# Optimization experiments

Measured on AMD Instinct MI355X. Metric: run time of the kernel, lower is better.

## Reference

```python
import jax, jax.numpy as jnp
import numpy as np

N_HEAD = 16


def setup_inputs() -> dict:
    key = jax.random.key(0)
    ks = jax.random.split(key, 5)
    B, L, C = 2, 2048, 1024
    s = 0.02
    return {
        "x": jax.random.normal(ks[0], (B, L, C), dtype=jnp.float32),
        "attn_mask": jnp.ones((B, L), dtype=jnp.int64),
        "Wq": jax.random.normal(ks[1], (C, C), dtype=jnp.float32) * s,
        "Wk": jax.random.normal(ks[2], (C, C), dtype=jnp.float32) * s,
        "Wv": jax.random.normal(ks[3], (C, C), dtype=jnp.float32) * s,
        "Wp": jax.random.normal(ks[4], (C, C), dtype=jnp.float32) * s,
    }


def reference(x, attn_mask, Wq, Wk, Wv, Wp):
    B, L, C = x.shape
    H = N_HEAD
    D = C // H
    # nn.Linear(bias=False): y = x @ W.T with W of shape (out, in)
    q = (x @ Wq.T).reshape(B, L, H, D).transpose(0, 2, 1, 3)  # (B,H,L,D)
    k = (x @ Wk.T).reshape(B, L, H, D).transpose(0, 2, 1, 3)
    v = (x @ Wv.T).reshape(B, L, H, D).transpose(0, 2, 1, 3)
    att = jnp.einsum("bhqd,bhkd->bhqk", q, k) / jnp.sqrt(jnp.asarray(D, x.dtype))
    causal = jnp.tril(jnp.ones((L, L), dtype=bool))  # (L,L)
    tok = (attn_mask != 0)[:, None, None, :]  # (B,1,1,L) key-side padding mask
    mask = causal[None, None, :, :] & tok
    att = jnp.where(mask, att, -jnp.inf)
    att = jax.nn.softmax(att, axis=-1)
    # dropout p=0.0 (eval): identity
    y = jnp.einsum("bhqk,bhkd->bhqd", att, v)
    y = y.transpose(0, 2, 1, 3).reshape(B, L, C)
    return y @ Wp.T
```

## Files before the change

kernel.cpp:

```cpp
#include <hip/hip_runtime.h>
#include <hip/hip_bf16.h>
#include <cstdint>

typedef _Float16 f16;
typedef _Float16 f16x4 __attribute__((ext_vector_type(4)));
typedef _Float16 f16x8 __attribute__((ext_vector_type(8)));
typedef float f32x4 __attribute__((ext_vector_type(4)));

#define LNEG (-1e30f)
#define EXP2(x) __builtin_amdgcn_exp2f(x)

__device__ __forceinline__ f32x4 mfma16(f16x8 a, f16x8 b, f32x4 c){
    return __builtin_amdgcn_mfma_f32_16x16x32_f16(a, b, c, 0, 0, 0);
}

__global__ __launch_bounds__(256) void cvt5(
    const float* __restrict__ x,  const float* __restrict__ wq,
    const float* __restrict__ wk, const float* __restrict__ wv,
    const float* __restrict__ wp, f16* __restrict__ dst, int nx8)
{
    int i = blockIdx.x * blockDim.x + threadIdx.x;
    const float* src; int off;
    if (i < nx8){ src = x; off = i; }
    else {
        int j = i - nx8;
        int s = j >> 17;
        off = j & 131071;
        src = (s == 0) ? wq : (s == 1) ? wk : (s == 2) ? wv : wp;
    }
    const float4* p = (const float4*)src + (size_t)off * 2;
    float4 v0 = p[0], v1 = p[1];
    f16x8 o = { (f16)v0.x, (f16)v0.y, (f16)v0.z, (f16)v0.w,
                (f16)v1.x, (f16)v1.y, (f16)v1.z, (f16)v1.w };
    *(f16x8*)&dst[(size_t)i * 8] = o;
}

template<typename OutT>
__global__ __launch_bounds__(256) void gemm_xwt(
    const f16* __restrict__ A, const f16* __restrict__ W0, size_t wstride,
    OutT* __restrict__ out0, size_t ostride, f16* __restrict__ vtout,
    int M, int N, int K)
{
    const int tid  = threadIdx.x;
    const int lane = tid & 63;
    const int w    = tid >> 6;
    const int wr   = w >> 1, wc = w & 1;
    const int m0   = blockIdx.y * 128;
    const int n0   = blockIdx.x * 128;
    const f16* Wz  = W0 + wstride * blockIdx.z;
    OutT* out      = out0 + ostride * blockIdx.z;

    __shared__ f16 At[2][128 * 64];
    __shared__ f16 Bt[2][128 * 64];

    f32x4 acc[4][4] = {};
    f16x8 avr[4], bvr[4];

    int srow[4], scolb[4], sswz[4];
    #pragma unroll
    for (int j = 0; j < 4; ++j){
        int off  = (j * 256 + tid) * 16;
        srow[j]  = off >> 7;
        scolb[j] = off & 127;
        sswz[j]  = srow[j] * 128 + (scolb[j] ^ ((srow[j] & 7) << 4));
    }

    #pragma unroll
    for (int j = 0; j < 4; ++j){
        avr[j] = *(const f16x8*)&A [(size_t)(m0 + srow[j]) * K + (scolb[j] >> 1)];
        bvr[j] = *(const f16x8*)&Wz[(size_t)(n0 + srow[j]) * K + (scolb[j] >> 1)];
    }
    #pragma unroll
    for (int j = 0; j < 4; ++j){
        *(f16x8*)((char*)At[0] + sswz[j]) = avr[j];
        *(f16x8*)((char*)Bt[0] + sswz[j]) = bvr[j];
    }
    __syncthreads();

    const int NT = K >> 6;
    for (int t = 0; t < NT; ++t){
        const int cur = t & 1;
        const bool pre = (t + 1 < NT);
        if (pre){
            const int k0 = (t + 1) << 6;
            #pragma unroll
            for (int j = 0; j < 4; ++j){
                avr[j] = *(const f16x8*)&A [(size_t)(m0 + srow[j]) * K + k0 + (scolb[j] >> 1)];
                bvr[j] = *(const f16x8*)&Wz[(size_t)(n0 + srow[j]) * K + k0 + (scolb[j] >> 1)];
            }
        }
        #pragma unroll
        for (int kk = 0; kk < 2; ++kk){
            f16x8 af[4], bf[4];
            #pragma unroll
            for (int mf = 0; mf < 4; ++mf){
                int row = wr * 64 + mf * 16 + (lane & 15);
                int cb  = (kk * 64 + 16 * (lane >> 4)) ^ ((row & 7) << 4);
                af[mf] = *(const f16x8*)((const char*)At[cur] + row * 128 + cb);
            }
            #pragma unroll
            for (int nf = 0; nf < 4; ++nf){
                int row = wc * 64 + nf * 16 + (lane & 15);
                int cb  = (kk * 64 + 16 * (lane >> 4)) ^ ((row & 7) << 4);
                bf[nf] = *(const f16x8*)((const char*)Bt[cur] + row * 128 + cb);
            }
            #pragma unroll
            for (int mf = 0; mf < 4; ++mf)
                #pragma unroll
                for (int nf = 0; nf < 4; ++nf)
                    acc[mf][nf] = mfma16(af[mf], bf[nf], acc[mf][nf]);
        }
        if (pre){
            const int nb = cur ^ 1;
            #pragma unroll
            for (int j = 0; j < 4; ++j){
                *(f16x8*)((char*)At[nb] + sswz[j]) = avr[j];
                *(f16x8*)((char*)Bt[nb] + sswz[j]) = bvr[j];
            }
        }
        __syncthreads();
    }

    if (vtout != nullptr && blockIdx.z == 2){
        #pragma unroll
        for (int mf = 0; mf < 4; ++mf)
            #pragma unroll
            for (int nf = 0; nf < 4; ++nf){
                int row = m0 + wr * 64 + mf * 16 + 4 * (lane >> 4);
                int col = n0 + wc * 64 + nf * 16 + (lane & 15);
                int bb = row >> 11, ll = row & 2047;
                int bh = bb * 16 + (col >> 6), dd = col & 63;
                f16x4 o = { (f16)acc[mf][nf][0], (f16)acc[mf][nf][1],
                            (f16)acc[mf][nf][2], (f16)acc[mf][nf][3] };
                *(f16x4*)&vtout[((size_t)(bh * 64 + dd)) * 2048 + ll] = o;
            }
    } else {
        #pragma unroll
        for (int mf = 0; mf < 4; ++mf)
            #pragma unroll
            for (int nf = 0; nf < 4; ++nf)
                #pragma unroll
                for (int r = 0; r < 4; ++r){
                    int row = m0 + wr * 64 + mf * 16 + 4 * (lane >> 4) + r;
                    int col = n0 + wc * 64 + nf * 16 + (lane & 15);
                    out[(size_t)row * N + col] = (OutT)acc[mf][nf][r];
                }
    }
}

__global__ __launch_bounds__(256, 4) void attn_fused(
    const f16* __restrict__ q, const f16* __restrict__ k,
    const f16* __restrict__ vt, const int* __restrict__ amask,
    f16* __restrict__ y, float* __restrict__ pO, float* __restrict__ pML)
{
    const int tid  = threadIdx.x;
    const int lane = tid & 63;
    const int w    = tid >> 6;
    const int g    = lane >> 4;
    const int qq   = lane & 15;

    const int lin = blockIdx.x;
    const int bh  = lin & 31;
    const int grp = lin >> 5;
    int qt, ktLo, ktHi, part; bool fin;
    if (grp < 4)      { qt = 19 - grp;  ktLo = 0;  ktHi = qt + 1; fin = true;  part = 0; }
    else if (grp < 16){ qt = 16 + grp;  ktLo = 0;  ktHi = 16;     fin = false; part = 0; }
    else if (grp < 28){ qt = 47 - grp;  ktLo = 16; ktHi = qt + 1; fin = false; part = 1; }
    else              { qt = 43 - grp;  ktLo = 0;  ktHi = qt + 1; fin = true;  part = 0; }

    const int b = bh >> 4, h = bh & 15;
    const int q0w = qt * 64 + w * 16;

    __shared__ char sK[2][64 * 128];
    __shared__ char sV[2][64 * 128];
    __shared__ char sP[4][16 * 128];

    const int srow = (tid * 2) >> 3;
    const int sc8a = (tid * 2) & 7, sc8b = sc8a + 1;
    const int swka = (sc8a * 16) ^ ((srow & 7) << 4);
    const int swkb = (sc8b * 16) ^ ((srow & 7) << 4);
    const f16* kbase  = k  + ((size_t)b * 2048) * 1024 + h * 64;
    const f16* vtbase = vt + (size_t)bh * 64 * 2048;

    const f16 qscale = (f16)(0.125f * 1.44269504088896f);
    f16x8 aq[2];
    #pragma unroll
    for (int f = 0; f < 2; ++f){
        aq[f] = *(const f16x8*)&q[((size_t)(b * 2048 + q0w + qq)) * 1024 + h * 64 + f * 32 + 8 * g];
        #pragma unroll
        for (int j = 0; j < 8; ++j) aq[f][j] *= qscale;
    }

    f32x4 acc_o[4] = {};
    float m_ln = LNEG, l_ln = 0.f;

    char* pbase = sP[w] + qq * 128;
    const int swp = (qq & 7) << 4;

    {
        const int k0p = ktLo * 64;
        f16x8 ka  = *(const f16x8*)(kbase  + (size_t)(k0p + srow) * 1024 + sc8a * 8);
        f16x8 kb2 = *(const f16x8*)(kbase  + (size_t)(k0p + srow) * 1024 + sc8b * 8);
        f16x8 va  = *(const f16x8*)(vtbase + (size_t)srow * 2048 + k0p + sc8a * 8);
        f16x8 vb  = *(const f16x8*)(vtbase + (size_t)srow * 2048 + k0p + sc8b * 8);
        *(f16x8*)(sK[0] + srow * 128 + swka) = ka;
        *(f16x8*)(sK[0] + srow * 128 + swkb) = kb2;
        *(f16x8*)(sV[0] + srow * 128 + swka) = va;
        *(f16x8*)(sV[0] + srow * 128 + swkb) = vb;
    }
    __syncthreads();

    for (int kt = ktLo; kt < ktHi; ++kt){
        const int cur = (kt - ktLo) & 1;
        const int k0 = kt * 64;
        const bool pre = (kt + 1 < ktHi);

        f16x8 ka, kb2, va, vb;
        if (pre){
            const int nk0 = k0 + 64;
            ka  = *(const f16x8*)(kbase  + (size_t)(nk0 + srow) * 1024 + sc8a * 8);
            kb2 = *(const f16x8*)(kbase  + (size_t)(nk0 + srow) * 1024 + sc8b * 8);
            va  = *(const f16x8*)(vtbase + (size_t)srow * 2048 + nk0 + sc8a * 8);
            vb  = *(const f16x8*)(vtbase + (size_t)srow * 2048 + nk0 + sc8b * 8);
        }

        unsigned long long tokbits = __ballot(amask[b * 2048 + k0 + lane] != 0);
        const bool tokall = (tokbits == ~0ull);

        f32x4 acc_s[4] = {};
        #pragma unroll
        for (int kf = 0; kf < 4; ++kf){
            const int keyl = kf * 16 + qq;
            const char* kr = sK[cur] + keyl * 128;
            const int sw = (keyl & 7) << 4;
            #pragma unroll
            for (int f = 0; f < 2; ++f){
                f16x8 ak = *(const f16x8*)(kr + ((f * 64 + 16 * g) ^ sw));
                acc_s[kf] = mfma16(ak, aq[f], acc_s[kf]);
            }
        }

        const bool fullt = (k0 + 63 <= q0w) && tokall;
        float sv[16];
        #pragma unroll
        for (int kf = 0; kf < 4; ++kf)
            #pragma unroll
            for (int r = 0; r < 4; ++r){
                float s = acc_s[kf][r];
                if (!fullt){
                    const int keyl = kf * 16 + 4 * g + r;
                    const bool ok = (k0 + keyl <= q0w + qq) && ((tokbits >> keyl) & 1);
                    s = ok ? s : LNEG;
                }
                sv[kf * 4 + r] = s;
            }

        float tmax = sv[0];
        #pragma unroll
        for (int i = 1; i < 16; ++i) tmax = fmaxf(tmax, sv[i]);
        tmax = fmaxf(tmax, __shfl_xor(tmax, 16));
        tmax = fmaxf(tmax, __shfl_xor(tmax, 32));
        const bool skip = __all(tmax <= m_ln + 8.f);
        float alpha = 1.f;
        if (!skip){
            const float newm = fmaxf(m_ln, tmax);
            alpha = EXP2(m_ln - newm);
            m_ln = newm;
        }
        float rs = 0.f;
        #pragma unroll
        for (int i = 0; i < 16; ++i){ sv[i] = EXP2(sv[i] - m_ln); rs += sv[i]; }
        rs += __shfl_xor(rs, 16);
        rs += __shfl_xor(rs, 32);
        l_ln = l_ln * alpha + rs;
        if (!skip){
            #pragma unroll
            for (int r = 0; r < 4; ++r){
                const float ar = __shfl(alpha, 4 * g + r);
                #pragma unroll
                for (int nf = 0; nf < 4; ++nf) acc_o[nf][r] *= ar;
            }
        }

        #pragma unroll
        for (int kf = 0; kf < 4; ++kf){
            f16x4 pk = { (f16)sv[kf*4+0], (f16)sv[kf*4+1], (f16)sv[kf*4+2], (f16)sv[kf*4+3] };
            *(f16x4*)(pbase + ((kf * 32 + 8 * g) ^ swp)) = pk;
        }
        __syncthreads();

        #pragma unroll
        for (int f = 0; f < 2; ++f){
            f16x8 ap = *(const f16x8*)(pbase + ((f * 64 + 16 * g) ^ swp));
            #pragma unroll
            for (int nf = 0; nf < 4; ++nf){
                const int d = nf * 16 + qq;
                f16x8 bv = *(const f16x8*)(sV[cur] + d * 128 + ((f * 64 + 16 * g) ^ ((d & 7) << 4)));
                acc_o[nf] = mfma16(ap, bv, acc_o[nf]);
            }
        }

        if (pre){
            const int nb = cur ^ 1;
            *(f16x8*)(sK[nb] + srow * 128 + swka) = ka;
            *(f16x8*)(sK[nb] + srow * 128 + swkb) = kb2;
            *(f16x8*)(sV[nb] + srow * 128 + swka) = va;
            *(f16x8*)(sV[nb] + srow * 128 + swkb) = vb;
        }
        __syncthreads();
    }

    if (fin){
        const float invl = 1.f / l_ln;
        #pragma unroll
        for (int r = 0; r < 4; ++r){
            const float ir = __shfl(invl, 4 * g + r);
            const int row = q0w + 4 * g + r;
            #pragma unroll
            for (int nf = 0; nf < 4; ++nf)
                y[((size_t)(b * 2048 + row)) * 1024 + h * 64 + nf * 16 + qq] = (f16)(acc_o[nf][r] * ir);
        }
    } else {
        const int qi = qt - 20;
        const size_t base = (((size_t)part * 12 + qi) * 32 + bh) * 64;
        #pragma unroll
        for (int r = 0; r < 4; ++r){
            const int row_local = w * 16 + 4 * g + r;
            float* po = pO + (base + row_local) * 64;
            #pragma unroll
            for (int nf = 0; nf < 4; ++nf)
                po[nf * 16 + qq] = acc_o[nf][r];
        }
        if (lane < 16){
            const size_t mlb = (base + w * 16 + lane) * 2;
            pML[mlb]     = m_ln;
            pML[mlb + 1] = l_ln;
        }
    }
}

__global__ __launch_bounds__(256) void attn_merge(
    const float* __restrict__ pO, const float* __restrict__ pML, f16* __restrict__ y)
{
    const int t = blockIdx.x * 256 + threadIdx.x;
    const int dc = (t & 3) * 16;
    const int rowg = t >> 2;
    const int row = rowg & 63;
    const int bh  = (rowg >> 6) & 31;
    const int qi  = rowg >> 11;
    const size_t rbase = ((size_t)qi * 32 + bh) * 64 + row;
    const size_t PST = (size_t)12 * 32 * 64;

    const float mA = pML[rbase * 2],         lA = pML[rbase * 2 + 1];
    const float mB = pML[(PST + rbase) * 2], lB = pML[(PST + rbase) * 2 + 1];
    const float m  = fmaxf(mA, mB);
    const float wA = EXP2(mA - m), wB = EXP2(mB - m);
    const float inv = 1.f / (wA * lA + wB * lB);

    const float4* oA = (const float4*)(pO + rbase * 64 + dc);
    const float4* oB = (const float4*)(pO + (PST * 64) + rbase * 64 + dc);
    float ov[16];
    #pragma unroll
    for (int j = 0; j < 4; ++j){
        float4 a = oA[j], bb4 = oB[j];
        ov[j*4+0] = (wA * a.x + wB * bb4.x) * inv;
        ov[j*4+1] = (wA * a.y + wB * bb4.y) * inv;
        ov[j*4+2] = (wA * a.z + wB * bb4.z) * inv;
        ov[j*4+3] = (wA * a.w + wB * bb4.w) * inv;
    }
    const int b = bh >> 4, h = bh & 15;
    const int grow = (20 + qi) * 64 + row;
    f16* yp = &y[((size_t)(b * 2048 + grow)) * 1024 + h * 64 + dc];
    f16x8 o0 = { (f16)ov[0],(f16)ov[1],(f16)ov[2],(f16)ov[3],(f16)ov[4],(f16)ov[5],(f16)ov[6],(f16)ov[7] };
    f16x8 o1 = { (f16)ov[8],(f16)ov[9],(f16)ov[10],(f16)ov[11],(f16)ov[12],(f16)ov[13],(f16)ov[14],(f16)ov[15] };
    *(f16x8*)yp = o0;
    *(f16x8*)(yp + 8) = o1;
}

extern "C" void kernel_launch(void* const* d_in, const int* in_sizes, int n_in,
                              void* d_out, int out_size, void* d_ws, size_t ws_size,
                              hipStream_t stream){
    const float* x  = (const float*)d_in[0];
    const int*   am = (const int*)d_in[1];
    const float* Wq = (const float*)d_in[2];
    const float* Wk = (const float*)d_in[3];
    const float* Wv = (const float*)d_in[4];
    const float* Wp = (const float*)d_in[5];
    float* out = (float*)d_out;

    char* ws = (char*)d_ws;
    const size_t XE = (size_t)4096 * 1024;
    const size_t WE = (size_t)1024 * 1024;

    f16* x16 = (f16*)(ws);
    f16* w16 = (f16*)(ws + XE * 2);
    f16* qkv = (f16*)(ws + XE * 2 + WE * 8);
    f16* vt  = (f16*)(ws + XE * 2 + WE * 8 + XE * 6);
    f16* y16 = (f16*)(ws + XE * 2 + WE * 8 + XE * 8);
    float* pO  = (float*)ws;
    float* pML = (float*)(ws + (size_t)2*12*32*64*64*4);

    cvt5<<<4096, 256, 0, stream>>>(x, Wq, Wk, Wv, Wp, x16, (int)(XE / 8));

    gemm_xwt<f16><<<dim3(8, 32, 3), 256, 0, stream>>>(x16, w16, WE, qkv, XE, vt, 4096, 1024, 1024);

    attn_fused<<<dim3(1408), 256, 0, stream>>>(qkv, qkv + XE, vt, am, y16, pO, pML);

    attn_merge<<<384, 256, 0, stream>>>(pO, pML, y16);

    gemm_xwt<float><<<dim3(8, 32, 1), 256, 0, stream>>>(y16, w16 + 3 * WE, 0, out, 0, nullptr, 4096, 1024, 1024);
}
```

Baseline: 110.7 us.

## Add 64-row tile output projection GEMM and relax P-tile barrier in attention

Replaces the output projection GEMM with a dedicated kernel using 64x128 tiles, doubling the block count to 512 for better CU occupancy on the small projection. Separately, the block-wide barrier after writing the P tile to shared memory in the attention loop becomes a local LDS wait plus scheduling barrier. That is only safe if each wave reads back only its own P rows. Smaller tiles lower per-block data reuse.

Result: no change. 108.6 us (median of 2 runs) (-1.9%).

```diff
diff --git a/kernel.cpp b/kernel.cpp
--- a/kernel.cpp
+++ b/kernel.cpp
@@ -148,6 +148,102 @@
     }
 }
 
+__global__ __launch_bounds__(256) void gemm_proj64(
+    const f16* __restrict__ A, const f16* __restrict__ W,
+    float* __restrict__ out, int M, int N, int K)
+{
+    const int tid  = threadIdx.x;
+    const int lane = tid & 63;
+    const int wc   = tid >> 6;
+    const int g    = lane >> 4;
+    const int qq   = lane & 15;
+    const int m0   = blockIdx.y * 64;
+    const int n0   = blockIdx.x * 128;
+
+    __shared__ f16 At[2][64 * 64];
+    __shared__ f16 Bt[2][128 * 64];
+
+    f32x4 acc[4][2] = {};
+    f16x8 avr[2], bvr[4];
+
+    int arow[2], acol[2], aswz[2];
+    #pragma unroll
+    for (int j = 0; j < 2; ++j){
+        int c  = j * 256 + tid;
+        arow[j] = c >> 3; acol[j] = (c & 7) * 8;
+        aswz[j] = arow[j] * 128 + (((c & 7) * 16) ^ ((arow[j] & 7) << 4));
+    }
+    int brow[4], bcol[4], bswz[4];
+    #pragma unroll
+    for (int j = 0; j < 4; ++j){
+        int c  = j * 256 + tid;
+        brow[j] = c >> 3; bcol[j] = (c & 7) * 8;
+        bswz[j] = brow[j] * 128 + (((c & 7) * 16) ^ ((brow[j] & 7) << 4));
+    }
+
+    #pragma unroll
+    for (int j = 0; j < 2; ++j) avr[j] = *(const f16x8*)&A[(size_t)(m0 + arow[j]) * K + acol[j]];
+    #pragma unroll
+    for (int j = 0; j < 4; ++j) bvr[j] = *(const f16x8*)&W[(size_t)(n0 + brow[j]) * K + bcol[j]];
+    #pragma unroll
+    for (int j = 0; j < 2; ++j) *(f16x8*)((char*)At[0] + aswz[j]) = avr[j];
+    #pragma unroll
+    for (int j = 0; j < 4; ++j) *(f16x8*)((char*)Bt[0] + bswz[j]) = bvr[j];
+    __syncthreads();
+
+    const int NT = K >> 6;
+    for (int t = 0; t < NT; ++t){
+        const int cur = t & 1;
+        const bool pre = (t + 1 < NT);
+        if (pre){
+            const int k0 = (t + 1) << 6;
+            #pragma unroll
+            for (int j = 0; j < 2; ++j) avr[j] = *(const f16x8*)&A[(size_t)(m0 + arow[j]) * K + k0 + acol[j]];
+            #pragma unroll
+            for (int j = 0; j < 4; ++j) bvr[j] = *(const f16x8*)&W[(size_t)(n0 + brow[j]) * K + k0 + bcol[j]];
+        }
+        #pragma unroll
+        for (int kk = 0; kk < 2; ++kk){
+            f16x8 af[4], bf[2];
+            #pragma unroll
+            for (int mf = 0; mf < 4; ++mf){
+                int row = mf * 16 + qq;
+                int cb  = (kk * 64 + 16 * g) ^ ((row & 7) << 4);
+                af[mf] = *(const f16x8*)((const char*)At[cur] + row * 128 + cb);
+            }
+            #pragma unroll
+            for (int nf = 0; nf < 2; ++nf){
+                int row = wc * 32 + nf * 16 + qq;
+                int cb  = (kk * 64 + 16 * g) ^ ((row & 7) << 4);
+                bf[nf] = *(const f16x8*)((const char*)Bt[cur] + row * 128 + cb);
+            }
+            #pragma unroll
+            for (int mf = 0; mf < 4; ++mf)
+                #pragma unroll
+                for (int nf = 0; nf < 2; ++nf)
+                    acc[mf][nf] = mfma16(af[mf], bf[nf], acc[mf][nf]);
+        }
+        if (pre){
+            const int nb = cur ^ 1;
+            #pragma unroll
+            for (int j = 0; j < 2; ++j) *(f16x8*)((char*)At[nb] + aswz[j]) = avr[j];
+            #pragma unroll
+            for (int j = 0; j < 4; ++j) *(f16x8*)((char*)Bt[nb] + bswz[j]) = bvr[j];
+        }
+        __syncthreads();
+    }
+    #pragma unroll
+    for (int mf = 0; mf < 4; ++mf)
+        #pragma unroll
+        for (int nf = 0; nf < 2; ++nf)
+            #pragma unroll
+            for (int r = 0; r < 4; ++r){
+                int row = m0 + mf * 16 + 4 * g + r;
+                int col = n0 + wc * 32 + nf * 16 + qq;
+                out[(size_t)row * N + col] = acc[mf][nf][r];
+            }
+}
+
 __global__ __launch_bounds__(256, 4) void attn_fused(
     const f16* __restrict__ q, const f16* __restrict__ k,
     const f16* __restrict__ vt, const int* __restrict__ amask,
@@ -287,7 +383,8 @@
             f16x4 pk = { (f16)sv[kf*4+0], (f16)sv[kf*4+1], (f16)sv[kf*4+2], (f16)sv[kf*4+3] };
             *(f16x4*)(pbase + ((kf * 32 + 8 * g) ^ swp)) = pk;
         }
-        __syncthreads();
+        asm volatile("s_waitcnt lgkmcnt(0)" ::: "memory");
+        __builtin_amdgcn_sched_barrier(0);
 
         #pragma unroll
         for (int f = 0; f < 2; ++f){
@@ -408,5 +505,5 @@
 
     attn_merge<<<384, 256, 0, stream>>>(pO, pML, y16);
 
-    gemm_xwt<float><<<dim3(8, 32, 1), 256, 0, stream>>>(y16, w16 + 3 * WE, 0, out, 0, nullptr, 4096, 1024, 1024);
-}
+    gemm_proj64<<<dim3(8, 64), 256, 0, stream>>>(y16, w16 + 3 * WE, out, 4096, 1024, 1024);
+}
```

## Shrink GEMM M-tile to 64 and replace attention P-store barrier with waitcnt

Applied to the files above, without the earlier changes.

Both GEMM launches now use a 64x128 block tile instead of 128x128. Each of the four waves computes a 64x32 slice, and the grid doubles along M, which gives more blocks and better CU fill on a wide GPU at the cost of less operand reuse per block. In the attention kernel, the __syncthreads after writing P to shared memory becomes an lgkmcnt wait plus a sched_barrier. This assumes each wave only reads back its own P rows, which saves a block-wide barrier per key tile but is only correct if no cross-wave data dependence exists.

Result: no change. 111.8 us (+1.0%).

```diff
diff --git a/kernel.cpp b/kernel.cpp
--- a/kernel.cpp
+++ b/kernel.cpp
@@ -36,45 +36,50 @@
 }
 
 template<typename OutT>
-__global__ __launch_bounds__(256) void gemm_xwt(
+__global__ __launch_bounds__(256) void gemm64(
     const f16* __restrict__ A, const f16* __restrict__ W0, size_t wstride,
     OutT* __restrict__ out0, size_t ostride, f16* __restrict__ vtout,
     int M, int N, int K)
 {
     const int tid  = threadIdx.x;
     const int lane = tid & 63;
-    const int w    = tid >> 6;
-    const int wr   = w >> 1, wc = w & 1;
-    const int m0   = blockIdx.y * 128;
+    const int wc   = tid >> 6;
+    const int g    = lane >> 4;
+    const int qq   = lane & 15;
+    const int m0   = blockIdx.y * 64;
     const int n0   = blockIdx.x * 128;
     const f16* Wz  = W0 + wstride * blockIdx.z;
     OutT* out      = out0 + ostride * blockIdx.z;
 
-    __shared__ f16 At[2][128 * 64];
+    __shared__ f16 At[2][64 * 64];
     __shared__ f16 Bt[2][128 * 64];
 
-    f32x4 acc[4][4] = {};
-    f16x8 avr[4], bvr[4];
-
-    int srow[4], scolb[4], sswz[4];
+    f32x4 acc[4][2] = {};
+    f16x8 avr[2], bvr[4];
+
+    int arow[2], acol[2], aswz[2];
+    #pragma unroll
+    for (int j = 0; j < 2; ++j){
+        int c  = j * 256 + tid;
+        arow[j] = c >> 3; acol[j] = (c & 7) * 8;
+        aswz[j] = arow[j] * 128 + (((c & 7) * 16) ^ ((arow[j] & 7) << 4));
+    }
+    int brow[4], bcol[4], bswz[4];
     #pragma unroll
     for (int j = 0; j < 4; ++j){
-        int off  = (j * 256 + tid) * 16;
-        srow[j]  = off >> 7;
-        scolb[j] = off & 127;
-        sswz[j]  = srow[j] * 128 + (scolb[j] ^ ((srow[j] & 7) << 4));
-    }
-
-    #pragma unroll
-    for (int j = 0; j < 4; ++j){
-        avr[j] = *(const f16x8*)&A [(size_t)(m0 + srow[j]) * K + (scolb[j] >> 1)];
-        bvr[j] = *(const f16x8*)&Wz[(size_t)(n0 + srow[j]) * K + (scolb[j] >> 1)];
-    }
-    #pragma unroll
-    for (int j = 0; j < 4; ++j){
-        *(f16x8*)((char*)At[0] + sswz[j]) = avr[j];
-        *(f16x8*)((char*)Bt[0] + sswz[j]) = bvr[j];
-    }
+        int c  = j * 256 + tid;
+        brow[j] = c >> 3; bcol[j] = (c & 7) * 8;
+        bswz[j] = brow[j] * 128 + (((c & 7) * 16) ^ ((brow[j] & 7) << 4));
+    }
+
+    #pragma unroll
+    for (int j = 0; j < 2; ++j) avr[j] = *(const f16x8*)&A [(size_t)(m0 + arow[j]) * K + acol[j]];
+    #pragma unroll
+    for (int j = 0; j < 4; ++j) bvr[j] = *(const f16x8*)&Wz[(size_t)(n0 + brow[j]) * K + bcol[j]];
+    #pragma unroll
+    for (int j = 0; j < 2; ++j) *(f16x8*)((char*)At[0] + aswz[j]) = avr[j];
+    #pragma unroll
+    for (int j = 0; j < 4; ++j) *(f16x8*)((char*)Bt[0] + bswz[j]) = bvr[j];
     __syncthreads();
 
     const int NT = K >> 6;
@@ -84,39 +89,37 @@
         if (pre){
             const int k0 = (t + 1) << 6;
             #pragma unroll
-            for (int j = 0; j < 4; ++j){
-                avr[j] = *(const f16x8*)&A [(size_t)(m0 + srow[j]) * K + k0 + (scolb[j] >> 1)];
-                bvr[j] = *(const f16x8*)&Wz[(size_t)(n0 + srow[j]) * K + k0 + (scolb[j] >> 1)];
-            }
+            for (int j = 0; j < 2; ++j) avr[j] = *(const f16x8*)&A [(size_t)(m0 + arow[j]) * K + k0 + acol[j]];
+            #pragma unroll
+            for (int j = 0; j < 4; ++j) bvr[j] = *(const f16x8*)&Wz[(size_t)(n0 + brow[j]) * K + k0 + bcol[j]];
         }
         #pragma unroll
         for (int kk = 0; kk < 2; ++kk){
-            f16x8 af[4], bf[4];
+            f16x8 af[4], bf[2];
             #pragma unroll
             for (int mf = 0; mf < 4; ++mf){
-                int row = wr * 64 + mf * 16 + (lane & 15);
-                int cb  = (kk * 64 + 16 * (lane >> 4)) ^ ((row & 7) << 4);
+                int row = mf * 16 + qq;
+                int cb  = (kk * 64 + 16 * g) ^ ((row & 7) << 4);
                 af[mf] = *(const f16x8*)((const char*)At[cur] + row * 128 + cb);
             }
             #pragma unroll
-            for (int nf = 0; nf < 4; ++nf){
-                int row = wc * 64 + nf * 16 + (lane & 15);
-                int cb  = (kk * 64 + 16 * (lane >> 4)) ^ ((row & 7) << 4);
+            for (int nf = 0; nf < 2; ++nf){
+                int row = wc * 32 + nf * 16 + qq;
+                int cb  = (kk * 64 + 16 * g) ^ ((row & 7) << 4);
                 bf[nf] = *(const f16x8*)((const char*)Bt[cur] + row * 128 + cb);
             }
             #pragma unroll
             for (int mf = 0; mf < 4; ++mf)
                 #pragma unroll
-                for (int nf = 0; nf < 4; ++nf)
+                for (int nf = 0; nf < 2; ++nf)
                     acc[mf][nf] = mfma16(af[mf], bf[nf], acc[mf][nf]);
         }
         if (pre){
             const int nb = cur ^ 1;
             #pragma unroll
-            for (int j = 0; j < 4; ++j){
-                *(f16x8*)((char*)At[nb] + sswz[j]) = avr[j];
-                *(f16x8*)((char*)Bt[nb] + sswz[j]) = bvr[j];
-            }
+            for (int j = 0; j < 2; ++j) *(f16x8*)((char*)At[nb] + aswz[j]) = avr[j];
+            #pragma unroll
+            for (int j = 0; j < 4; ++j) *(f16x8*)((char*)Bt[nb] + bswz[j]) = bvr[j];
         }
         __syncthreads();
     }
@@ -125,9 +128,9 @@
         #pragma unroll
         for (int mf = 0; mf < 4; ++mf)
             #pragma unroll
-            for (int nf = 0; nf < 4; ++nf){
-                int row = m0 + wr * 64 + mf * 16 + 4 * (lane >> 4);
-                int col = n0 + wc * 64 + nf * 16 + (lane & 15);
+            for (int nf = 0; nf < 2; ++nf){
+                int row = m0 + mf * 16 + 4 * g;
+                int col = n0 + wc * 32 + nf * 16 + qq;
                 int bb = row >> 11, ll = row & 2047;
                 int bh = bb * 16 + (col >> 6), dd = col & 63;
                 f16x4 o = { (f16)acc[mf][nf][0], (f16)acc[mf][nf][1],
@@ -138,11 +141,11 @@
         #pragma unroll
         for (int mf = 0; mf < 4; ++mf)
             #pragma unroll
-            for (int nf = 0; nf < 4; ++nf)
+            for (int nf = 0; nf < 2; ++nf)
                 #pragma unroll
                 for (int r = 0; r < 4; ++r){
-                    int row = m0 + wr * 64 + mf * 16 + 4 * (lane >> 4) + r;
-                    int col = n0 + wc * 64 + nf * 16 + (lane & 15);
+                    int row = m0 + mf * 16 + 4 * g + r;
+                    int col = n0 + wc * 32 + nf * 16 + qq;
                     out[(size_t)row * N + col] = (OutT)acc[mf][nf][r];
                 }
     }
@@ -287,7 +290,8 @@
             f16x4 pk = { (f16)sv[kf*4+0], (f16)sv[kf*4+1], (f16)sv[kf*4+2], (f16)sv[kf*4+3] };
             *(f16x4*)(pbase + ((kf * 32 + 8 * g) ^ swp)) = pk;
         }
-        __syncthreads();
+        asm volatile("s_waitcnt lgkmcnt(0)" ::: "memory");
+        __builtin_amdgcn_sched_barrier(0);
 
         #pragma unroll
         for (int f = 0; f < 2; ++f){
@@ -402,11 +406,11 @@
 
     cvt5<<<4096, 256, 0, stream>>>(x, Wq, Wk, Wv, Wp, x16, (int)(XE / 8));
 
-    gemm_xwt<f16><<<dim3(8, 32, 3), 256, 0, stream>>>(x16, w16, WE, qkv, XE, vt, 4096, 1024, 1024);
+    gemm64<f16><<<dim3(8, 64, 3), 256, 0, stream>>>(x16, w16, WE, qkv, XE, vt, 4096, 1024, 1024);
 
     attn_fused<<<dim3(1408), 256, 0, stream>>>(qkv, qkv + XE, vt, am, y16, pO, pML);
 
     attn_merge<<<384, 256, 0, stream>>>(pO, pML, y16);
 
-    gemm_xwt<float><<<dim3(8, 32, 1), 256, 0, stream>>>(y16, w16 + 3 * WE, 0, out, 0, nullptr, 4096, 1024, 1024);
-}
+    gemm64<float><<<dim3(8, 64, 1), 256, 0, stream>>>(y16, w16 + 3 * WE, 0, out, 0, nullptr, 4096, 1024, 1024);
+}
```
